# Kernel tuning notes

Hardware: AMD Instinct MI355X
Metric: run time of the kernel (lower is better)

Reference implementation:

```python
import jax, jax.numpy as jnp
import numpy as np

B, S, H = 2, 1024, 1024
NH, NKV, DH = 16, 4, 64
I, E, TOPK = 4096, 8, 2
EPS = 1e-5
ROPE_THETA = 10000.0


def setup_inputs() -> dict:
    key = jax.random.key(0)
    ks = jax.random.split(key, 16)
    std = 0.02
    inp = {
        'hidden_states': jax.random.normal(ks[0], (B, S, H), jnp.float32),
        'attention_mask': jnp.ones((B, S), jnp.int32),
        'position_ids': jnp.broadcast_to(jnp.arange(S, dtype=jnp.int32), (B, S)),
        'q_w': jax.random.normal(ks[1], (H, NH * DH), jnp.float32) * std,
        'k_w': jax.random.normal(ks[2], (H, NKV * DH), jnp.float32) * std,
        'v_w': jax.random.normal(ks[3], (H, NKV * DH), jnp.float32) * std,
        'o_w': jax.random.normal(ks[4], (NH * DH, H), jnp.float32) * std,
        'pre_attn_scale': jnp.ones((H,), jnp.float32),
        'post_attn_scale': jnp.ones((H,), jnp.float32),
        'pre_moe_scale': jnp.ones((H,), jnp.float32),
        'post_moe_scale': jnp.ones((H,), jnp.float32),
        'gate_w': jax.random.normal(ks[5], (H, E), jnp.float32) * std,
        'w_in': jax.random.normal(ks[6], (E, H, I), jnp.float32) * std,
        'w_v': jax.random.normal(ks[7], (E, H, I), jnp.float32) * std,
        'w_out': jax.random.normal(ks[8], (E, I, H), jnp.float32) * std,
    }
    return inp


def _rmsnorm(x, scale):
    var = jnp.mean(jnp.square(x), axis=-1, keepdims=True)
    return x * jax.lax.rsqrt(var + EPS) * scale


def _rope(x, positions):
    # x: [B, S, nheads, DH]; rotate-half RoPE
    half = DH // 2
    inv_freq = 1.0 / (ROPE_THETA ** (jnp.arange(0, half, dtype=jnp.float32) / half))
    ang = positions.astype(jnp.float32)[..., None] * inv_freq  # [B,S,half]
    cos = jnp.cos(ang)[:, :, None, :]
    sin = jnp.sin(ang)[:, :, None, :]
    x1, x2 = x[..., :half], x[..., half:]
    return jnp.concatenate([x1 * cos - x2 * sin, x2 * cos + x1 * sin], axis=-1)


def _attention(x, attention_mask, position_ids, q_w, k_w, v_w, o_w):
    q = (x @ q_w).reshape(B, S, NH, DH)
    k = (x @ k_w).reshape(B, S, NKV, DH)
    v = (x @ v_w).reshape(B, S, NKV, DH)
    q = _rope(q, position_ids)
    k = _rope(k, position_ids)
    groups = NH // NKV
    k = jnp.repeat(k, groups, axis=2)  # [B,S,NH,DH]
    v = jnp.repeat(v, groups, axis=2)
    scale = DH ** -0.5
    scores = jnp.einsum('bqhd,bkhd->bhqk', q, k) * scale
    causal = jnp.tril(jnp.ones((S, S), bool))
    valid = causal[None, None] & (attention_mask[:, None, None, :] > 0)
    scores = jnp.where(valid, scores, jnp.float32(-1e9))
    probs = jax.nn.softmax(scores, axis=-1)
    out = jnp.einsum('bhqk,bkhd->bqhd', probs, v).reshape(B, S, NH * DH)
    return out @ o_w


def _moe(x, gate_w, w_in, w_v, w_out):
    xf = x.reshape(-1, H)  # [T,H]
    T = xf.shape[0]
    logits = xf @ gate_w  # [T,E]
    probs = jax.nn.softmax(logits, axis=-1)
    top_w, top_i = jax.lax.top_k(probs, TOPK)  # Grok-1: no renormalization
    cw = jnp.zeros((T, E), xf.dtype).at[jnp.arange(T)[:, None], top_i].add(top_w)
    out = jnp.zeros_like(xf)
    for e in range(E):  # fixed small loop over experts
        h = jax.nn.gelu(xf @ w_in[e]) * (xf @ w_v[e])
        out = out + cw[:, e:e + 1] * (h @ w_out[e])
    return out.reshape(x.shape)


def reference(hidden_states, attention_mask, position_ids, q_w, k_w, v_w, o_w,
              pre_attn_scale, post_attn_scale, pre_moe_scale, post_moe_scale,
              gate_w, w_in, w_v, w_out):
    h = _rmsnorm(hidden_states, pre_attn_scale)
    attn = _attention(h, attention_mask, position_ids, q_w, k_w, v_w, o_w)
    attn = _rmsnorm(attn, post_attn_scale)
    x = hidden_states + attn
    h2 = _rmsnorm(x, pre_moe_scale)
    moe = _moe(h2, gate_w, w_in, w_v, w_out)
    moe = _rmsnorm(moe, post_moe_scale)
    return x + moe
```

## Files before the change

kernel.cpp:

```cpp
#include <hip/hip_runtime.h>
#include <hip/hip_bf16.h>
#include <math.h>

namespace {

constexpr int BB=2, SS=1024, HH=1024, NH=16, NKV=4, DH=64;
constexpr int II=4096, EE=8;
constexpr int TT=BB*SS;
constexpr int QKV=1536;
constexpr float EPS=1e-5f;

typedef __bf16 bf16x8 __attribute__((ext_vector_type(8)));
typedef float f32x4 __attribute__((ext_vector_type(4)));

__device__ __forceinline__ unsigned short f2bf(float x){
  union { float f; unsigned u; } un; un.f = x;
  unsigned r = un.u + 0x7fffu + ((un.u>>16)&1u);
  return (unsigned short)(r>>16);
}
__device__ __forceinline__ float bfval(unsigned short h){
  union { unsigned u; float f; } r; r.u = ((unsigned)h)<<16; return r.f;
}
__device__ __forceinline__ void split2(float v, unsigned short& hi, unsigned short& lo){
  hi = f2bf(v);
  lo = f2bf(v - bfval(hi));
}

__device__ __forceinline__ void gl_lds16(const void* g, void* l){
  __builtin_amdgcn_global_load_lds(
    (const __attribute__((address_space(1))) unsigned int*)g,
    (__attribute__((address_space(3))) unsigned int*)l, 16, 0, 0);
}

__device__ __forceinline__ float gelu_tanh(float x){
  float x3 = x*x*x;
  return 0.5f*x*(1.f + tanhf(0.7978845608028654f*(x + 0.044715f*x3)));
}

__global__ void rmsnorm_kernel(const float* __restrict__ in, const float* __restrict__ scale,
                               float* __restrict__ outf, unsigned short* __restrict__ outb,
                               unsigned short* __restrict__ outh, unsigned short* __restrict__ outl){
  int row = blockIdx.x, tid = threadIdx.x;
  const float* x = in + (size_t)row*HH;
  float ss = 0.f;
  for (int i=tid;i<HH;i+=256){ float v=x[i]; ss+=v*v; }
  __shared__ float red[256];
  red[tid]=ss; __syncthreads();
  for (int s=128;s>0;s>>=1){ if(tid<s) red[tid]+=red[tid+s]; __syncthreads(); }
  float inv = rsqrtf(red[0]/(float)HH + EPS);
  for (int i=tid;i<HH;i+=256){
    float v = x[i]*inv*scale[i];
    size_t o = (size_t)row*HH+i;
    if (outf) outf[o]=v;
    if (outb) outb[o]=f2bf(v);
    if (outh){ unsigned short h,l; split2(v,h,l); outh[o]=h; outl[o]=l; }
  }
}

__global__ void fuse_attn_post(const float* __restrict__ ao_raw, const float* __restrict__ hidden,
                               const float* __restrict__ post_scale, const float* __restrict__ pre_scale,
                               float* __restrict__ xb, float* __restrict__ hn,
                               unsigned short* __restrict__ hnb){
  int row = blockIdx.x, tid = threadIdx.x;
  const float* a = ao_raw + (size_t)row*HH;
  const float* h = hidden + (size_t)row*HH;
  float av[4], hv[4];
  float ss = 0.f;
#pragma unroll
  for (int i=0;i<4;i++){
    int idx = tid + i*256;
    av[i]=a[idx]; hv[i]=h[idx];
    ss += av[i]*av[i];
  }
  __shared__ float red[256];
  red[tid]=ss; __syncthreads();
  for (int s=128;s>0;s>>=1){ if(tid<s) red[tid]+=red[tid+s]; __syncthreads(); }
  float inv1 = rsqrtf(red[0]/(float)HH + EPS);
  __syncthreads();
  float xv[4]; float ss2=0.f;
#pragma unroll
  for (int i=0;i<4;i++){
    int idx = tid + i*256;
    xv[i] = hv[i] + av[i]*inv1*post_scale[idx];
    ss2 += xv[i]*xv[i];
  }
  red[tid]=ss2; __syncthreads();
  for (int s=128;s>0;s>>=1){ if(tid<s) red[tid]+=red[tid+s]; __syncthreads(); }
  float inv2 = rsqrtf(red[0]/(float)HH + EPS);
#pragma unroll
  for (int i=0;i<4;i++){
    int idx = tid + i*256;
    size_t o = (size_t)row*HH + idx;
    xb[o] = xv[i];
    float v = xv[i]*inv2*pre_scale[idx];
    hn[o] = v;
    hnb[o] = f2bf(v);
  }
}

__global__ void fuse_moe_post(const float* __restrict__ moe, const float* __restrict__ xb,
                              const float* __restrict__ scale, float* __restrict__ out){
  int row = blockIdx.x, tid = threadIdx.x;
  const float* m = moe + (size_t)row*HH;
  float mv[4]; float ss=0.f;
#pragma unroll
  for (int i=0;i<4;i++){
    int idx = tid + i*256;
    mv[i]=m[idx]; ss += mv[i]*mv[i];
  }
  __shared__ float red[256];
  red[tid]=ss; __syncthreads();
  for (int s=128;s>0;s>>=1){ if(tid<s) red[tid]+=red[tid+s]; __syncthreads(); }
  float inv = rsqrtf(red[0]/(float)HH + EPS);
#pragma unroll
  for (int i=0;i<4;i++){
    int idx = tid + i*256;
    size_t o = (size_t)row*HH + idx;
    out[o] = xb[o] + mv[i]*inv*scale[idx];
  }
}

__global__ void rope_split_kernel(const float* __restrict__ x, int stride, int off,
                                  const int* __restrict__ pos_ids,
                                  unsigned short* __restrict__ oh, unsigned short* __restrict__ ol,
                                  int nheads){
  int idx = blockIdx.x*256 + threadIdx.x;
  int total = TT*nheads*32;
  if (idx >= total) return;
  int j = idx & 31;
  int hh = (idx>>5) % nheads;
  int t = idx / (32*nheads);
  float pos = (float)pos_ids[t];
  float inv_freq = powf(10000.f, -(float)j/32.f);
  float ang = pos * inv_freq;
  float s, c; sincosf(ang, &s, &c);
  const float* p = x + (size_t)t*stride + off + hh*DH;
  float x1 = p[j], x2 = p[j+32];
  float r1 = x1*c - x2*s;
  float r2 = x2*c + x1*s;
  size_t o = ((size_t)t*nheads + hh)*DH;
  unsigned short h1,l1,h2,l2;
  split2(r1,h1,l1); split2(r2,h2,l2);
  oh[o+j]=h1;    ol[o+j]=l1;
  oh[o+j+32]=h2; ol[o+j+32]=l2;
}

__global__ __launch_bounds__(256) void vt_split_kernel(const float* __restrict__ src, int stride, int off,
    unsigned short* __restrict__ vth, unsigned short* __restrict__ vtl){
  int k0 = blockIdx.x*64;
  int kvh = blockIdx.y;
  int b = blockIdx.z;
  __shared__ float tile[64][65];
  int t = threadIdx.x;
  int c4 = (t&15)*4, gg = t>>4;
#pragma unroll
  for (int r=0;r<4;r++){
    int kk = gg + r*16;
    float4 v = *reinterpret_cast<const float4*>(src + (size_t)(b*SS+k0+kk)*stride + off + kvh*DH + c4);
    tile[kk][c4]=v.x; tile[kk][c4+1]=v.y; tile[kk][c4+2]=v.z; tile[kk][c4+3]=v.w;
  }
  __syncthreads();
#pragma unroll
  for (int r=0;r<4;r++){
    int dd = gg + r*16;
    ushort4 h4, l4v;
    split2(tile[c4  ][dd], h4.x, l4v.x);
    split2(tile[c4+1][dd], h4.y, l4v.y);
    split2(tile[c4+2][dd], h4.z, l4v.z);
    split2(tile[c4+3][dd], h4.w, l4v.w);
    size_t o = ((size_t)(b*NKV+kvh)*DH + dd)*SS + k0 + c4;
    *reinterpret_cast<ushort4*>(vth+o)=h4;
    *reinterpret_cast<ushort4*>(vtl+o)=l4v;
  }
}

__global__ __launch_bounds__(256) void attn_mfma(
    const unsigned short* __restrict__ qh, const unsigned short* __restrict__ ql,
    const unsigned short* __restrict__ khp, const unsigned short* __restrict__ klp,
    const unsigned short* __restrict__ vth, const unsigned short* __restrict__ vtl,
    const int* __restrict__ amask,
    unsigned short* __restrict__ ctxh, unsigned short* __restrict__ ctxl)
{
  int qb = blockIdx.x, h = blockIdx.y, b = blockIdx.z;
  int kvh = h >> 2;
  int tid = threadIdx.x;
  int w = tid >> 6, lane = tid & 63;
  int g = lane >> 4, l15 = lane & 15;

  __shared__ __align__(16) unsigned short Klh[64*64];
  __shared__ __align__(16) unsigned short Kll[64*64];
  __shared__ __align__(16) unsigned short Vlh[64*64];
  __shared__ __align__(16) unsigned short Vll[64*64];
  __shared__ __align__(16) unsigned short Pst[4][2][16*72];

  int q0w = qb*64 + w*16;

  bf16x8 qfh[2], qfl[2];
  {
    size_t qrow = ((size_t)(b*SS + q0w + l15)*NH + h)*DH;
#pragma unroll
    for (int ks=0; ks<2; ks++){
      qfh[ks] = *reinterpret_cast<const bf16x8*>(qh + qrow + ks*32 + g*8);
      qfl[ks] = *reinterpret_cast<const bf16x8*>(ql + qrow + ks*32 + g*8);
    }
  }

  f32x4 acc[4];
  float m_run[4], l_run[4];
#pragma unroll
  for (int i=0;i<4;i++){ acc[i]=f32x4{0,0,0,0}; m_run[i]=-1e30f; l_run[i]=0.f; }

  int nkv = qb + 1;
  for (int kblk=0; kblk<nkv; kblk++){
    int k0 = kblk*64;
    __syncthreads();
#pragma unroll
    for (int shot=0; shot<2; shot++){
      int a = shot*256 + tid;
      int row = a>>3, seg = a&7;
      int ss8 = (seg ^ (row&7))*8;
      int lo = row*64 + seg*8;
      size_t kg = ((size_t)(b*SS + k0 + row)*NKV + kvh)*DH + ss8;
      size_t vg = ((size_t)(b*NKV + kvh)*DH + row)*SS + k0 + ss8;
      gl_lds16(khp + kg, Klh + lo);
      gl_lds16(klp + kg, Kll + lo);
      gl_lds16(vth + vg, Vlh + lo);
      gl_lds16(vtl + vg, Vll + lo);
    }
    __syncthreads();

    f32x4 sf[4];
#pragma unroll
    for (int nf=0;nf<4;nf++) sf[nf]=f32x4{0,0,0,0};
#pragma unroll
    for (int ks=0; ks<2; ks++){
#pragma unroll
      for (int nf=0; nf<4; nf++){
        int krow = nf*16 + l15;
        int off = krow*64 + (((ks*4+g) ^ (krow&7))*8);
        bf16x8 bh = *reinterpret_cast<const bf16x8*>(Klh + off);
        bf16x8 bl = *reinterpret_cast<const bf16x8*>(Kll + off);
        sf[nf] = __builtin_amdgcn_mfma_f32_16x16x32_bf16(qfh[ks], bh, sf[nf],0,0,0);
        sf[nf] = __builtin_amdgcn_mfma_f32_16x16x32_bf16(qfh[ks], bl, sf[nf],0,0,0);
        sf[nf] = __builtin_amdgcn_mfma_f32_16x16x32_bf16(qfl[ks], bh, sf[nf],0,0,0);
      }
    }

    int am4[4];
#pragma unroll
    for (int nf=0;nf<4;nf++) am4[nf] = amask[b*SS + k0 + nf*16 + l15];
#pragma unroll
    for (int nf=0;nf<4;nf++){
      int k_abs = k0 + nf*16 + l15;
#pragma unroll
      for (int r=0;r<4;r++){
        float s = sf[nf][r]*0.125f;
        int q_abs = q0w + g*4 + r;
        if (k_abs > q_abs || am4[nf] <= 0) s = -1e9f;
        sf[nf][r] = s;
      }
    }

    float m_new[4], fsc[4];
#pragma unroll
    for (int r=0;r<4;r++){
      float v = fmaxf(fmaxf(sf[0][r],sf[1][r]), fmaxf(sf[2][r],sf[3][r]));
#pragma unroll
      for (int o=1;o<16;o<<=1) v = fmaxf(v, __shfl_xor(v,o));
      m_new[r] = fmaxf(m_run[r], v);
      fsc[r] = expf(m_run[r] - m_new[r]);
      m_run[r] = m_new[r];
    }

    unsigned short* Ph  = Pst[w][0];
    unsigned short* Plo = Pst[w][1];
    float rsum[4] = {0.f,0.f,0.f,0.f};
#pragma unroll
    for (int nf=0;nf<4;nf++){
#pragma unroll
      for (int r=0;r<4;r++){
        float p = expf(sf[nf][r] - m_new[r]);
        rsum[r] += p;
        unsigned short hi = f2bf(p);
        float lo = p - bfval(hi);
        Ph [(g*4+r)*72 + nf*16 + l15] = hi;
        Plo[(g*4+r)*72 + nf*16 + l15] = f2bf(lo);
      }
    }
#pragma unroll
    for (int r=0;r<4;r++){
#pragma unroll
      for (int o=1;o<16;o<<=1) rsum[r] += __shfl_xor(rsum[r],o);
      l_run[r] = l_run[r]*fsc[r] + rsum[r];
#pragma unroll
      for (int nf=0;nf<4;nf++) acc[nf][r] *= fsc[r];
    }

#pragma unroll
    for (int ks=0; ks<2; ks++){
      bf16x8 pa = *reinterpret_cast<const bf16x8*>(Ph  + l15*72 + ks*32 + g*8);
      bf16x8 pl = *reinterpret_cast<const bf16x8*>(Plo + l15*72 + ks*32 + g*8);
#pragma unroll
      for (int nf=0; nf<4; nf++){
        int drow = nf*16 + l15;
        int off = drow*64 + (((ks*4+g) ^ (drow&7))*8);
        bf16x8 vh = *reinterpret_cast<const bf16x8*>(Vlh + off);
        bf16x8 vl = *reinterpret_cast<const bf16x8*>(Vll + off);
        acc[nf] = __builtin_amdgcn_mfma_f32_16x16x32_bf16(pa, vh, acc[nf],0,0,0);
        acc[nf] = __builtin_amdgcn_mfma_f32_16x16x32_bf16(pa, vl, acc[nf],0,0,0);
        acc[nf] = __builtin_amdgcn_mfma_f32_16x16x32_bf16(pl, vh, acc[nf],0,0,0);
      }
    }
  }

#pragma unroll
  for (int r=0;r<4;r++){
    float inv = 1.f / l_run[r];
    size_t orow = ((size_t)(b*SS + q0w + g*4 + r)*NH + h)*DH;
#pragma unroll
    for (int nf=0;nf<4;nf++){
      float v = acc[nf][r]*inv;
      unsigned short hi,lo; split2(v,hi,lo);
      ctxh[orow + nf*16 + l15] = hi;
      ctxl[orow + nf*16 + l15] = lo;
    }
  }
}

__global__ void route_kernel(const float* __restrict__ x, const float* __restrict__ gw,
                             int* __restrict__ counts, int* __restrict__ lists,
                             float* __restrict__ cw){
  int t = blockIdx.x;
  int lane = threadIdx.x;
  float acc[EE];
#pragma unroll
  for (int e=0;e<EE;e++) acc[e]=0.f;
  for (int hh=lane; hh<HH; hh+=64){
    float xv = x[(size_t)t*HH + hh];
#pragma unroll
    for (int e=0;e<EE;e++) acc[e] += xv*gw[hh*EE+e];
  }
#pragma unroll
  for (int e=0;e<EE;e++){
#pragma unroll
    for (int off=1; off<64; off<<=1) acc[e] += __shfl_xor(acc[e], off);
  }
  if (lane==0){
    float m = acc[0];
    for (int e=1;e<EE;e++) m = fmaxf(m, acc[e]);
    float p[EE], s=0.f;
    for (int e=0;e<EE;e++){ p[e]=expf(acc[e]-m); s+=p[e]; }
    float invs = 1.f/s;
    for (int e=0;e<EE;e++) p[e]*=invs;
    int i1=0;
    for (int e=1;e<EE;e++) if (p[e]>p[i1]) i1=e;
    int i2 = (i1==0)?1:0;
    for (int e=0;e<EE;e++) if (e!=i1 && p[e]>p[i2]) i2=e;
    int pos = atomicAdd(&counts[i1],1);
    lists[i1*TT+pos]=t; cw[i1*TT+pos]=p[i1];
    pos = atomicAdd(&counts[i2],1);
    lists[i2*TT+pos]=t; cw[i2*TT+pos]=p[i2];
  }
}

__global__ void prefix_kernel(const int* __restrict__ c, int* __restrict__ b,
                              const float* __restrict__ cw, float* __restrict__ cw_slot){
  int lane = threadIdx.x;
  __shared__ int sb[EE+1];
  if (lane==0){
    int s=0;
    for (int e=0;e<EE;e++){ sb[e]=s; b[e]=s; s+=c[e]; }
    sb[EE]=s; b[EE]=s;
  }
  __syncthreads();
  for (int e=0;e<EE;e++){
    int cnt=c[e], base=sb[e];
    for (int i=lane;i<cnt;i+=64) cw_slot[base+i]=cw[e*TT+i];
  }
}

__global__ void moe_combine(const unsigned short* __restrict__ t0,
                            const unsigned short* __restrict__ t1,
                            const float* __restrict__ cwslot,
                            const int* __restrict__ ntotp,
                            unsigned short* __restrict__ ehb){
  int row = blockIdx.x;
  if (row >= *ntotp) return;
  float c = cwslot[row];
  size_t base = (size_t)row*II;
  int tid = threadIdx.x;
  for (int c0 = tid*8; c0 < II; c0 += 256*8){
    ushort4 x0 = *reinterpret_cast<const ushort4*>(t0+base+c0);
    ushort4 x1 = *reinterpret_cast<const ushort4*>(t0+base+c0+4);
    ushort4 y0 = *reinterpret_cast<const ushort4*>(t1+base+c0);
    ushort4 y1 = *reinterpret_cast<const ushort4*>(t1+base+c0+4);
    ushort4 o0, o1;
    o0.x = f2bf(gelu_tanh(bfval(x0.x))*bfval(y0.x)*c);
    o0.y = f2bf(gelu_tanh(bfval(x0.y))*bfval(y0.y)*c);
    o0.z = f2bf(gelu_tanh(bfval(x0.z))*bfval(y0.z)*c);
    o0.w = f2bf(gelu_tanh(bfval(x0.w))*bfval(y0.w)*c);
    o1.x = f2bf(gelu_tanh(bfval(x1.x))*bfval(y1.x)*c);
    o1.y = f2bf(gelu_tanh(bfval(x1.y))*bfval(y1.y)*c);
    o1.z = f2bf(gelu_tanh(bfval(x1.z))*bfval(y1.z)*c);
    o1.w = f2bf(gelu_tanh(bfval(x1.w))*bfval(y1.w)*c);
    *reinterpret_cast<ushort4*>(ehb+base+c0)   = o0;
    *reinterpret_cast<ushort4*>(ehb+base+c0+4) = o1;
  }
}

__global__ __launch_bounds__(256) void transpose_cvt(const float* __restrict__ in,
    unsigned short* __restrict__ out, int K, int N, size_t in_zstride, size_t out_zstride){
  __shared__ float tile[64][65];
  int k0 = blockIdx.x*64, n0 = blockIdx.y*64;
  const float* inz = in + in_zstride*blockIdx.z;
  unsigned short* outz = out + out_zstride*blockIdx.z;
  int t = threadIdx.x;
  int c4 = (t&15)*4, g = t>>4;
#pragma unroll
  for (int r=0;r<4;r++){
    int kk = g + r*16;
    float4 v = *reinterpret_cast<const float4*>(inz + (size_t)(k0+kk)*N + n0 + c4);
    tile[kk][c4]=v.x; tile[kk][c4+1]=v.y; tile[kk][c4+2]=v.z; tile[kk][c4+3]=v.w;
  }
  __syncthreads();
#pragma unroll
  for (int r=0;r<4;r++){
    int nn = g + r*16;
    ushort4 o;
    o.x=f2bf(tile[c4][nn]);   o.y=f2bf(tile[c4+1][nn]);
    o.z=f2bf(tile[c4+2][nn]); o.w=f2bf(tile[c4+3][nn]);
    *reinterpret_cast<ushort4*>(outz + (size_t)(n0+nn)*K + k0 + c4) = o;
  }
}

__global__ __launch_bounds__(256) void transpose_cvt_split(const float* __restrict__ in,
    unsigned short* __restrict__ oh, unsigned short* __restrict__ ol, int K, int N){
  __shared__ float tile[64][65];
  int k0 = blockIdx.x*64, n0 = blockIdx.y*64;
  int t = threadIdx.x;
  int c4 = (t&15)*4, g = t>>4;
#pragma unroll
  for (int r=0;r<4;r++){
    int kk = g + r*16;
    float4 v = *reinterpret_cast<const float4*>(in + (size_t)(k0+kk)*N + n0 + c4);
    tile[kk][c4]=v.x; tile[kk][c4+1]=v.y; tile[kk][c4+2]=v.z; tile[kk][c4+3]=v.w;
  }
  __syncthreads();
#pragma unroll
  for (int r=0;r<4;r++){
    int nn = g + r*16;
    ushort4 h4, l4v;
    split2(tile[c4  ][nn], h4.x, l4v.x);
    split2(tile[c4+1][nn], h4.y, l4v.y);
    split2(tile[c4+2][nn], h4.z, l4v.z);
    split2(tile[c4+3][nn], h4.w, l4v.w);
    size_t o = (size_t)(n0+nn)*K + k0 + c4;
    *reinterpret_cast<ushort4*>(oh + o) = h4;
    *reinterpret_cast<ushort4*>(ol + o) = l4v;
  }
}

__global__ __launch_bounds__(256,2) void mgemm_split(
    const unsigned short* __restrict__ Ah, const unsigned short* __restrict__ Alo,
    const unsigned short* __restrict__ Bh, const unsigned short* __restrict__ Blo,
    float* __restrict__ Cf, int NY, int N, int K)
{
  int bid = blockIdx.x;
  int qq = bid >> 7, rr = bid & 127;
  int xti = rr >> 3, sbit = rr & 7;
  int g = qq*8 + sbit;
  if (g >= NY) return;
  int row0 = xti*128, col0 = g*128;
  __shared__ __align__(16) unsigned short lds[32768];

  int t = threadIdx.x;
  int lane = t&63, w = t>>6, wr = w>>1, wc = w&1;
  int sr = t>>2, seg = t&3;
  int swzs = (t>>3)&3;

  f32x4 acc[4][4];
#pragma unroll
  for (int m=0;m<4;m++)
#pragma unroll
    for (int n=0;n<4;n++) acc[m][n]=f32x4{0,0,0,0};

  int l15 = lane&15, l4 = lane>>4;
  int swzr = (l15>>1)&3;

  auto stage = [&](int buf, int k0){
    unsigned short* Lb = lds + buf*16384;
    int ksw = (seg ^ swzs)*8;
#pragma unroll
    for (int i=0;i<2;i++){
      int ldso = (sr + i*64)*32 + seg*8;
      size_t ar = (size_t)(row0 + sr + i*64);
      size_t br = (size_t)(col0 + sr + i*64);
      gl_lds16(Ah  + ar*K + k0 + ksw, Lb +         ldso);
      gl_lds16(Alo + ar*K + k0 + ksw, Lb + 4096  + ldso);
      gl_lds16(Bh  + br*K + k0 + ksw, Lb + 8192  + ldso);
      gl_lds16(Blo + br*K + k0 + ksw, Lb + 12288 + ldso);
    }
  };

  stage(0, 0);
  __syncthreads();
  int cur = 0;
  int NIT = K/32;
  int cofs = (l4 ^ swzr)*8;
  for (int it=0; it<NIT; it++){
    if (it+1 < NIT) stage(cur^1, (it+1)*32);
    const unsigned short* Lb = lds + cur*16384;
    bf16x8 ah[4], al[4], bh[4], bl[4];
#pragma unroll
    for (int m=0;m<4;m++){
      int ro = (wr*64 + m*16 + l15)*32 + cofs;
      ah[m]=*reinterpret_cast<const bf16x8*>(Lb +        ro);
      al[m]=*reinterpret_cast<const bf16x8*>(Lb + 4096 + ro);
    }
#pragma unroll
    for (int n=0;n<4;n++){
      int ro = (wc*64 + n*16 + l15)*32 + cofs;
      bh[n]=*reinterpret_cast<const bf16x8*>(Lb + 8192  + ro);
      bl[n]=*reinterpret_cast<const bf16x8*>(Lb + 12288 + ro);
    }
#pragma unroll
    for (int m=0;m<4;m++)
#pragma unroll
      for (int n=0;n<4;n++){
        acc[m][n] = __builtin_amdgcn_mfma_f32_16x16x32_bf16(ah[m], bh[n], acc[m][n], 0,0,0);
        acc[m][n] = __builtin_amdgcn_mfma_f32_16x16x32_bf16(ah[m], bl[n], acc[m][n], 0,0,0);
        acc[m][n] = __builtin_amdgcn_mfma_f32_16x16x32_bf16(al[m], bh[n], acc[m][n], 0,0,0);
      }
    __syncthreads();
    cur ^= 1;
  }

#pragma unroll
  for (int m=0;m<4;m++){
    int rb = wr*64 + m*16 + l4*4;
#pragma unroll
    for (int n=0;n<4;n++){
      int col = col0 + wc*64 + n*16 + l15;
#pragma unroll
      for (int r=0;r<4;r++){
        int row = row0 + rb + r;
        Cf[(size_t)row*N + col] = acc[m][n][r];
      }
    }
  }
}

__global__ __launch_bounds__(256,2) void mgemm_up(
    const unsigned short* __restrict__ A, const unsigned short* __restrict__ B0b,
    const unsigned short* __restrict__ B1b, size_t bstride,
    unsigned short* __restrict__ Cb0, unsigned short* __restrict__ Cb1,
    const int* __restrict__ listb,
    const int* __restrict__ countb, const int* __restrict__ basep)
{
  int bid = blockIdx.x;
  int qq = bid >> 7, rr = bid & 127;
  int xti = rr >> 3, sbit = rr & 7;
  int g = qq*8 + sbit;
  int y = g & 31, e = g >> 5;

  int M = countb[e];
  int row0 = xti*128;
  if (row0 >= M) return;
  int which = y & 1;
  int col0 = (y >> 1)*256;
  const unsigned short* B = (which ? B1b : B0b) + bstride*e;
  int slot = basep[e];
  const int* rowlist = listb + e*TT;

  __shared__ __align__(16) unsigned short lds[3][12288];

  int t = threadIdx.x;
  int lane = t&63, w = t>>6;
  int sr = t>>2, seg = t&3;
  int swzs = (t>>3)&3;

  size_t arow[2], brow[4];
#pragma unroll
  for (int i=0;i<2;i++){
    int r = row0 + sr + i*64;
    int rc = (r < M) ? r : (M-1);
    arow[i] = (size_t)rowlist[rc];
  }
#pragma unroll
  for (int i=0;i<4;i++)
    brow[i] = (size_t)(col0 + sr + i*64);

  f32x4 acc[8][4];
#pragma unroll
  for (int m=0;m<8;m++)
#pragma unroll
    for (int n=0;n<4;n++) acc[m][n]=f32x4{0,0,0,0};

  int l15 = lane&15, l4 = lane>>4;
  int cofs = (l4 ^ ((l15>>1)&3))*8;

  auto stage = [&](int buf, int k0){
    int ksw = (seg ^ swzs)*8;
#pragma unroll
    for (int i=0;i<2;i++){
      int ldso = (sr + i*64)*32 + seg*8;
      gl_lds16(A + arow[i]*HH + k0 + ksw, &lds[buf][0] + ldso);
    }
#pragma unroll
    for (int i=0;i<4;i++){
      int ldso = 4096 + (sr + i*64)*32 + seg*8;
      gl_lds16(B + brow[i]*HH + k0 + ksw, &lds[buf][0] + ldso);
    }
  };

  constexpr int NIT = HH/32;
  stage(0, 0);
  stage(1, 32);

  for (int it=0; it<NIT; it++){
    if (it+1 < NIT) asm volatile("s_waitcnt vmcnt(6)" ::: "memory");
    else            asm volatile("s_waitcnt vmcnt(0)" ::: "memory");
    __builtin_amdgcn_s_barrier();
    if (it+2 < NIT) stage((it+2)%3, (it+2)*32);

    const unsigned short* La = &lds[it%3][0];
    const unsigned short* Lb = La + 4096;
    bf16x8 af[8], bf[4];
#pragma unroll
    for (int m=0;m<8;m++)
      af[m] = *reinterpret_cast<const bf16x8*>(La + (m*16 + l15)*32 + cofs);
#pragma unroll
    for (int n=0;n<4;n++)
      bf[n] = *reinterpret_cast<const bf16x8*>(Lb + (w*64 + n*16 + l15)*32 + cofs);
#pragma unroll
    for (int m=0;m<8;m++)
#pragma unroll
      for (int n=0;n<4;n++)
        acc[m][n] = __builtin_amdgcn_mfma_f32_16x16x32_bf16(af[m], bf[n], acc[m][n], 0,0,0);
  }

  unsigned short* Cb = which ? Cb1 : Cb0;
#pragma unroll
  for (int m=0;m<8;m++){
    int rb = m*16 + l4*4;
#pragma unroll
    for (int n=0;n<4;n++){
      int col = col0 + w*64 + n*16 + l15;
#pragma unroll
      for (int r=0;r<4;r++){
        int row = row0 + rb + r;
        if (row >= M) continue;
        Cb[(size_t)(slot+row)*II + col] = f2bf(acc[m][n][r]);
      }
    }
  }
}

__global__ __launch_bounds__(256,3) void mgemm_down(
    const unsigned short* __restrict__ A, const unsigned short* __restrict__ B0b,
    size_t bstride, float* __restrict__ Cf,
    const int* __restrict__ listb,
    const int* __restrict__ countb, const int* __restrict__ basep)
{
  int bid = blockIdx.x;
  int qq = bid >> 7, rr = bid & 127;
  int xti = rr >> 3, sbit = rr & 7;
  int g = qq*8 + sbit;
  int y = g & 15, e = g >> 4;

  int M = countb[e];
  int row0 = xti*128;
  if (row0 >= M) return;
  int col0 = (y & 7)*128;
  int kbase = (y >> 3)*(II/2);
  int KL = II/2;
  const unsigned short* B = B0b + bstride*e;
  int slot = basep[e];
  const int* rowlist = listb + e*TT;

  __shared__ __align__(16) unsigned short lds[3][2][4096];

  int t = threadIdx.x;
  int lane = t&63, w = t>>6, wr = w>>1, wc = w&1;
  int sr = t>>2, seg = t&3;
  int swzs = (t>>3)&3;

  size_t arow[2], brow[2];
#pragma unroll
  for (int i=0;i<2;i++){
    int r = row0 + sr + i*64;
    int rc = (r < M) ? r : (M-1);
    arow[i] = (size_t)(slot + rc);
    brow[i] = (size_t)(col0 + sr + i*64);
  }

  f32x4 acc[4][4];
#pragma unroll
  for (int m=0;m<4;m++)
#pragma unroll
    for (int n=0;n<4;n++) acc[m][n]=f32x4{0,0,0,0};

  int l15 = lane&15, l4 = lane>>4;
  int cofs = (l4 ^ ((l15>>1)&3))*8;

  auto stage = [&](int buf, int k0){
    int ksw = (seg ^ swzs)*8;
#pragma unroll
    for (int i=0;i<2;i++){
      int ldso = (sr + i*64)*32 + seg*8;
      gl_lds16(A + arow[i]*II + kbase + k0 + ksw, &lds[buf][0][0] + ldso);
      gl_lds16(B + brow[i]*II + kbase + k0 + ksw, &lds[buf][1][0] + ldso);
    }
  };

  int NIT = KL/32;
  stage(0, 0);
  stage(1, 32);

  for (int it=0; it<NIT; it++){
    if (it+1 < NIT) asm volatile("s_waitcnt vmcnt(4)" ::: "memory");
    else            asm volatile("s_waitcnt vmcnt(0)" ::: "memory");
    __builtin_amdgcn_s_barrier();
    if (it+2 < NIT) stage((it+2)%3, (it+2)*32);

    int cb = it%3;
    const unsigned short* La = &lds[cb][0][0];
    const unsigned short* Lb = &lds[cb][1][0];
    bf16x8 af[4], bf[4];
#pragma unroll
    for (int m=0;m<4;m++)
      af[m] = *reinterpret_cast<const bf16x8*>(La + (wr*64 + m*16 + l15)*32 + cofs);
#pragma unroll
    for (int n=0;n<4;n++)
      bf[n] = *reinterpret_cast<const bf16x8*>(Lb + (wc*64 + n*16 + l15)*32 + cofs);
#pragma unroll
    for (int m=0;m<4;m++)
#pragma unroll
      for (int n=0;n<4;n++)
        acc[m][n] = __builtin_amdgcn_mfma_f32_16x16x32_bf16(af[m], bf[n], acc[m][n], 0,0,0);
  }

#pragma unroll
  for (int m=0;m<4;m++){
    int rb = wr*64 + m*16 + l4*4;
#pragma unroll
    for (int n=0;n<4;n++){
      int col = col0 + wc*64 + n*16 + l15;
#pragma unroll
      for (int r=0;r<4;r++){
        int row = row0 + rb + r;
        if (row >= M) continue;
        atomicAdd(&Cf[(size_t)rowlist[row]*HH + col], acc[m][n][r]);
      }
    }
  }
}

}

extern "C" void kernel_launch(void* const* d_in, const int* in_sizes, int n_in,
                              void* d_out, int out_size, void* d_ws, size_t ws_size,
                              hipStream_t stream) {
  const float* hidden = (const float*)d_in[0];
  const int*   mask   = (const int*)d_in[1];
  const int*   pos    = (const int*)d_in[2];
  const float* q_w    = (const float*)d_in[3];
  const float* k_w    = (const float*)d_in[4];
  const float* v_w    = (const float*)d_in[5];
  const float* o_w    = (const float*)d_in[6];
  const float* pre_attn_scale  = (const float*)d_in[7];
  const float* post_attn_scale = (const float*)d_in[8];
  const float* pre_moe_scale   = (const float*)d_in[9];
  const float* post_moe_scale  = (const float*)d_in[10];
  const float* gate_w = (const float*)d_in[11];
  const float* w_in   = (const float*)d_in[12];
  const float* w_v    = (const float*)d_in[13];
  const float* w_out  = (const float*)d_in[14];
  float* out = (float*)d_out;

  char* base = (char*)d_ws;
  auto carve = [&](size_t bytes)->char*{
    char* r = base; base += (bytes + 255) & ~(size_t)255; return r;
  };
  float* hn  = (float*)carve((size_t)TT*HH*4);
  unsigned short* hnb = (unsigned short*)carve((size_t)TT*HH*2);
  unsigned short* hnh = (unsigned short*)carve((size_t)TT*HH*2);
  unsigned short* hnl = (unsigned short*)carve((size_t)TT*HH*2);
  float* qkvb = (float*)carve((size_t)TT*QKV*4);
  unsigned short* qsh = (unsigned short*)carve((size_t)TT*NH*DH*2);
  unsigned short* qsl = (unsigned short*)carve((size_t)TT*NH*DH*2);
  unsigned short* ksh = (unsigned short*)carve((size_t)TT*NKV*DH*2);
  unsigned short* ksl = (unsigned short*)carve((size_t)TT*NKV*DH*2);
  unsigned short* vth = (unsigned short*)carve((size_t)TT*NKV*DH*2);
  unsigned short* vtl = (unsigned short*)carve((size_t)TT*NKV*DH*2);
  unsigned short* ctxh = (unsigned short*)carve((size_t)TT*NH*DH*2);
  unsigned short* ctxl = (unsigned short*)carve((size_t)TT*NH*DH*2);
  float* ao  = (float*)carve((size_t)TT*HH*4);
  float* xb  = (float*)carve((size_t)TT*HH*4);
  float* moe = (float*)carve((size_t)TT*HH*4);
  float* cw  = (float*)carve((size_t)EE*TT*4);
  float* cw_slot = (float*)carve((size_t)2*TT*4);
  int* counts = (int*)carve(64*4);
  int* bases  = (int*)carve(64*4);
  int* lists  = (int*)carve((size_t)EE*TT*4);
  unsigned short* qkvwTh = (unsigned short*)carve((size_t)QKV*HH*2);
  unsigned short* qkvwTl = (unsigned short*)carve((size_t)QKV*HH*2);
  unsigned short* owTh = (unsigned short*)carve((size_t)NH*DH*HH*2);
  unsigned short* owTl = (unsigned short*)carve((size_t)NH*DH*HH*2);
  unsigned short* ehb   = (unsigned short*)carve((size_t)2*TT*II*2);
  unsigned short* tmp0  = (unsigned short*)carve((size_t)2*TT*II*2);
  unsigned short* tmp1  = (unsigned short*)carve((size_t)2*TT*II*2);
  unsigned short* winT  = (unsigned short*)carve((size_t)EE*II*HH*2);
  unsigned short* wvT   = (unsigned short*)carve((size_t)EE*II*HH*2);
  unsigned short* woutT = (unsigned short*)carve((size_t)EE*HH*II*2);
  size_t estride = (size_t)II*HH;

  rmsnorm_kernel<<<TT,256,0,stream>>>(hidden, pre_attn_scale, nullptr, nullptr, hnh, hnl);
  transpose_cvt_split<<<dim3(16,16),256,0,stream>>>(q_w, qkvwTh, qkvwTl, HH, NH*DH);
  transpose_cvt_split<<<dim3(16,4), 256,0,stream>>>(k_w, qkvwTh + (size_t)1024*HH, qkvwTl + (size_t)1024*HH, HH, NKV*DH);
  transpose_cvt_split<<<dim3(16,4), 256,0,stream>>>(v_w, qkvwTh + (size_t)1280*HH, qkvwTl + (size_t)1280*HH, HH, NKV*DH);
  transpose_cvt_split<<<dim3(16,16),256,0,stream>>>(o_w, owTh, owTl, NH*DH, HH);

  mgemm_split<<<2*128,256,0,stream>>>(hnh, hnl, qkvwTh, qkvwTl, qkvb, QKV/128, QKV, HH);

  rope_split_kernel<<<(TT*NH*32+255)/256,256,0,stream>>>(qkvb, QKV, 0, pos, qsh, qsl, NH);
  rope_split_kernel<<<(TT*NKV*32+255)/256,256,0,stream>>>(qkvb, QKV, 1024, pos, ksh, ksl, NKV);
  vt_split_kernel<<<dim3(SS/64,NKV,BB),256,0,stream>>>(qkvb, QKV, 1280, vth, vtl);

  attn_mfma<<<dim3(SS/64,NH,BB),256,0,stream>>>(qsh, qsl, ksh, ksl, vth, vtl, mask, ctxh, ctxl);

  mgemm_split<<<128,256,0,stream>>>(ctxh, ctxl, owTh, owTl, ao, HH/128, HH, NH*DH);
  fuse_attn_post<<<TT,256,0,stream>>>(ao, hidden, post_attn_scale, pre_moe_scale, xb, hn, hnb);

  hipMemsetAsync(counts, 0, 64*sizeof(int), stream);
  hipMemsetAsync(moe, 0, (size_t)TT*HH*sizeof(float), stream);
  route_kernel<<<TT,64,0,stream>>>(hn, gate_w, counts, lists, cw);
  prefix_kernel<<<1,64,0,stream>>>(counts, bases, cw, cw_slot);

  transpose_cvt<<<dim3(16,64,EE),256,0,stream>>>(w_in, winT, HH, II, (size_t)HH*II, estride);
  transpose_cvt<<<dim3(16,64,EE),256,0,stream>>>(w_v,  wvT,  HH, II, (size_t)HH*II, estride);
  transpose_cvt<<<dim3(64,16,EE),256,0,stream>>>(w_out, woutT, II, HH, (size_t)II*HH, estride);

  mgemm_up<<<16*32*EE,256,0,stream>>>(hnb, winT, wvT, estride, tmp0, tmp1,
      lists, counts, bases);
  moe_combine<<<2*TT,256,0,stream>>>(tmp0, tmp1, cw_slot, bases+EE, ehb);
  mgemm_down<<<16*16*EE,256,0,stream>>>(ehb, woutT, estride, moe,
      lists, counts, bases);

  fuse_moe_post<<<TT,256,0,stream>>>(moe, xb, post_moe_scale, out);
}
```

Before: 602.8 us.

## Fuse GELU-gate combine into MoE up-projection GEMM epilogue

The MoE up-projection GEMM now computes both the w_in and w_v products for the same 128x128 tile in one block, keeping two accumulator sets. Its epilogue applies gelu(a)*b*routing weight and writes ehb directly. This removes the separate moe_combine kernel, the two bf16 intermediate buffers, and the cw_slot compaction step. In exchange the per-thread accumulators double and the tile shape changes from 128x256 to 128x128 per output, which may hurt occupancy or MFMA reuse.

```diff
diff --git a/kernel.cpp b/kernel.cpp
--- a/kernel.cpp
+++ b/kernel.cpp
@@ -363,48 +363,11 @@
   }
 }
 
-__global__ void prefix_kernel(const int* __restrict__ c, int* __restrict__ b,
-                              const float* __restrict__ cw, float* __restrict__ cw_slot){
-  int lane = threadIdx.x;
-  __shared__ int sb[EE+1];
-  if (lane==0){
+__global__ void prefix_kernel(const int* __restrict__ c, int* __restrict__ b){
+  if (threadIdx.x==0){
     int s=0;
-    for (int e=0;e<EE;e++){ sb[e]=s; b[e]=s; s+=c[e]; }
-    sb[EE]=s; b[EE]=s;
-  }
-  __syncthreads();
-  for (int e=0;e<EE;e++){
-    int cnt=c[e], base=sb[e];
-    for (int i=lane;i<cnt;i+=64) cw_slot[base+i]=cw[e*TT+i];
-  }
-}
-
-__global__ void moe_combine(const unsigned short* __restrict__ t0,
-                            const unsigned short* __restrict__ t1,
-                            const float* __restrict__ cwslot,
-                            const int* __restrict__ ntotp,
-                            unsigned short* __restrict__ ehb){
-  int row = blockIdx.x;
-  if (row >= *ntotp) return;
-  float c = cwslot[row];
-  size_t base = (size_t)row*II;
-  int tid = threadIdx.x;
-  for (int c0 = tid*8; c0 < II; c0 += 256*8){
-    ushort4 x0 = *reinterpret_cast<const ushort4*>(t0+base+c0);
-    ushort4 x1 = *reinterpret_cast<const ushort4*>(t0+base+c0+4);
-    ushort4 y0 = *reinterpret_cast<const ushort4*>(t1+base+c0);
-    ushort4 y1 = *reinterpret_cast<const ushort4*>(t1+base+c0+4);
-    ushort4 o0, o1;
-    o0.x = f2bf(gelu_tanh(bfval(x0.x))*bfval(y0.x)*c);
-    o0.y = f2bf(gelu_tanh(bfval(x0.y))*bfval(y0.y)*c);
-    o0.z = f2bf(gelu_tanh(bfval(x0.z))*bfval(y0.z)*c);
-    o0.w = f2bf(gelu_tanh(bfval(x0.w))*bfval(y0.w)*c);
-    o1.x = f2bf(gelu_tanh(bfval(x1.x))*bfval(y1.x)*c);
-    o1.y = f2bf(gelu_tanh(bfval(x1.y))*bfval(y1.y)*c);
-    o1.z = f2bf(gelu_tanh(bfval(x1.z))*bfval(y1.z)*c);
-    o1.w = f2bf(gelu_tanh(bfval(x1.w))*bfval(y1.w)*c);
-    *reinterpret_cast<ushort4*>(ehb+base+c0)   = o0;
-    *reinterpret_cast<ushort4*>(ehb+base+c0+4) = o1;
+    for (int e=0;e<EE;e++){ b[e]=s; s+=c[e]; }
+    b[EE]=s;
   }
 }
 
@@ -553,8 +516,8 @@
 __global__ __launch_bounds__(256,2) void mgemm_up(
     const unsigned short* __restrict__ A, const unsigned short* __restrict__ B0b,
     const unsigned short* __restrict__ B1b, size_t bstride,
-    unsigned short* __restrict__ Cb0, unsigned short* __restrict__ Cb1,
-    const int* __restrict__ listb,
+    unsigned short* __restrict__ ehb,
+    const int* __restrict__ listb, const float* __restrict__ cwb,
     const int* __restrict__ countb, const int* __restrict__ basep)
 {
   int bid = blockIdx.x;
@@ -566,35 +529,34 @@
   int M = countb[e];
   int row0 = xti*128;
   if (row0 >= M) return;
-  int which = y & 1;
-  int col0 = (y >> 1)*256;
-  const unsigned short* B = (which ? B1b : B0b) + bstride*e;
+  int col0 = y*128;
+  const unsigned short* B0 = B0b + bstride*e;
+  const unsigned short* B1 = B1b + bstride*e;
   int slot = basep[e];
   const int* rowlist = listb + e*TT;
-
-  __shared__ __align__(16) unsigned short lds[3][12288];
+  const float* cwp = cwb + e*TT;
+
+  __shared__ __align__(16) unsigned short lds[3][3][4096];
 
   int t = threadIdx.x;
-  int lane = t&63, w = t>>6;
+  int lane = t&63, w = t>>6, wr = w>>1, wc = w&1;
   int sr = t>>2, seg = t&3;
   int swzs = (t>>3)&3;
 
-  size_t arow[2], brow[4];
+  size_t arow[2], brow[2];
 #pragma unroll
   for (int i=0;i<2;i++){
     int r = row0 + sr + i*64;
     int rc = (r < M) ? r : (M-1);
     arow[i] = (size_t)rowlist[rc];
-  }
-#pragma unroll
-  for (int i=0;i<4;i++)
     brow[i] = (size_t)(col0 + sr + i*64);
-
-  f32x4 acc[8][4];
-#pragma unroll
-  for (int m=0;m<8;m++)
-#pragma unroll
-    for (int n=0;n<4;n++) acc[m][n]=f32x4{0,0,0,0};
+  }
+
+  f32x4 acc0[4][4], acc1[4][4];
+#pragma unroll
+  for (int m=0;m<4;m++)
+#pragma unroll
+    for (int n=0;n<4;n++){ acc0[m][n]=f32x4{0,0,0,0}; acc1[m][n]=f32x4{0,0,0,0}; }
 
   int l15 = lane&15, l4 = lane>>4;
   int cofs = (l4 ^ ((l15>>1)&3))*8;
@@ -604,12 +566,9 @@
 #pragma unroll
     for (int i=0;i<2;i++){
       int ldso = (sr + i*64)*32 + seg*8;
-      gl_lds16(A + arow[i]*HH + k0 + ksw, &lds[buf][0] + ldso);
-    }
-#pragma unroll
-    for (int i=0;i<4;i++){
-      int ldso = 4096 + (sr + i*64)*32 + seg*8;
-      gl_lds16(B + brow[i]*HH + k0 + ksw, &lds[buf][0] + ldso);
+      gl_lds16(A  + arow[i]*HH + k0 + ksw, &lds[buf][0][0] + ldso);
+      gl_lds16(B0 + brow[i]*HH + k0 + ksw, &lds[buf][1][0] + ldso);
+      gl_lds16(B1 + brow[i]*HH + k0 + ksw, &lds[buf][2][0] + ldso);
     }
   };
 
@@ -623,34 +582,41 @@
     __builtin_amdgcn_s_barrier();
     if (it+2 < NIT) stage((it+2)%3, (it+2)*32);
 
-    const unsigned short* La = &lds[it%3][0];
-    const unsigned short* Lb = La + 4096;
-    bf16x8 af[8], bf[4];
-#pragma unroll
-    for (int m=0;m<8;m++)
-      af[m] = *reinterpret_cast<const bf16x8*>(La + (m*16 + l15)*32 + cofs);
-#pragma unroll
-    for (int n=0;n<4;n++)
-      bf[n] = *reinterpret_cast<const bf16x8*>(Lb + (w*64 + n*16 + l15)*32 + cofs);
-#pragma unroll
-    for (int m=0;m<8;m++)
-#pragma unroll
-      for (int n=0;n<4;n++)
-        acc[m][n] = __builtin_amdgcn_mfma_f32_16x16x32_bf16(af[m], bf[n], acc[m][n], 0,0,0);
-  }
-
-  unsigned short* Cb = which ? Cb1 : Cb0;
-#pragma unroll
-  for (int m=0;m<8;m++){
-    int rb = m*16 + l4*4;
+    int cb = it%3;
+    const unsigned short* La  = &lds[cb][0][0];
+    const unsigned short* Lb0 = &lds[cb][1][0];
+    const unsigned short* Lb1 = &lds[cb][2][0];
+    bf16x8 af[4], b0f[4], b1f[4];
+#pragma unroll
+    for (int m=0;m<4;m++)
+      af[m] = *reinterpret_cast<const bf16x8*>(La + (wr*64 + m*16 + l15)*32 + cofs);
 #pragma unroll
     for (int n=0;n<4;n++){
-      int col = col0 + w*64 + n*16 + l15;
+      int ro = (wc*64 + n*16 + l15)*32 + cofs;
+      b0f[n] = *reinterpret_cast<const bf16x8*>(Lb0 + ro);
+      b1f[n] = *reinterpret_cast<const bf16x8*>(Lb1 + ro);
+    }
+#pragma unroll
+    for (int m=0;m<4;m++)
+#pragma unroll
+      for (int n=0;n<4;n++){
+        acc0[m][n] = __builtin_amdgcn_mfma_f32_16x16x32_bf16(af[m], b0f[n], acc0[m][n], 0,0,0);
+        acc1[m][n] = __builtin_amdgcn_mfma_f32_16x16x32_bf16(af[m], b1f[n], acc1[m][n], 0,0,0);
+      }
+  }
+
+#pragma unroll
+  for (int m=0;m<4;m++){
+    int rb = wr*64 + m*16 + l4*4;
+#pragma unroll
+    for (int n=0;n<4;n++){
+      int col = col0 + wc*64 + n*16 + l15;
 #pragma unroll
       for (int r=0;r<4;r++){
         int row = row0 + rb + r;
         if (row >= M) continue;
-        Cb[(size_t)(slot+row)*II + col] = f2bf(acc[m][n][r]);
+        float v = gelu_tanh(acc0[m][n][r]) * acc1[m][n][r] * cwp[row];
+        ehb[(size_t)(slot+row)*II + col] = f2bf(v);
       }
     }
   }
@@ -799,7 +765,6 @@
   float* xb  = (float*)carve((size_t)TT*HH*4);
   float* moe = (float*)carve((size_t)TT*HH*4);
   float* cw  = (float*)carve((size_t)EE*TT*4);
-  float* cw_slot = (float*)carve((size_t)2*TT*4);
   int* counts = (int*)carve(64*4);
   int* bases  = (int*)carve(64*4);
   int* lists  = (int*)carve((size_t)EE*TT*4);
@@ -808,8 +773,6 @@
   unsigned short* owTh = (unsigned short*)carve((size_t)NH*DH*HH*2);
   unsigned short* owTl = (unsigned short*)carve((size_t)NH*DH*HH*2);
   unsigned short* ehb   = (unsigned short*)carve((size_t)2*TT*II*2);
-  unsigned short* tmp0  = (unsigned short*)carve((size_t)2*TT*II*2);
-  unsigned short* tmp1  = (unsigned short*)carve((size_t)2*TT*II*2);
   unsigned short* winT  = (unsigned short*)carve((size_t)EE*II*HH*2);
   unsigned short* wvT   = (unsigned short*)carve((size_t)EE*II*HH*2);
   unsigned short* woutT = (unsigned short*)carve((size_t)EE*HH*II*2);
@@ -835,15 +798,14 @@
   hipMemsetAsync(counts, 0, 64*sizeof(int), stream);
   hipMemsetAsync(moe, 0, (size_t)TT*HH*sizeof(float), stream);
   route_kernel<<<TT,64,0,stream>>>(hn, gate_w, counts, lists, cw);
-  prefix_kernel<<<1,64,0,stream>>>(counts, bases, cw, cw_slot);
+  prefix_kernel<<<1,64,0,stream>>>(counts, bases);
 
   transpose_cvt<<<dim3(16,64,EE),256,0,stream>>>(w_in, winT, HH, II, (size_t)HH*II, estride);
   transpose_cvt<<<dim3(16,64,EE),256,0,stream>>>(w_v,  wvT,  HH, II, (size_t)HH*II, estride);
   transpose_cvt<<<dim3(64,16,EE),256,0,stream>>>(w_out, woutT, II, HH, (size_t)II*HH, estride);
 
-  mgemm_up<<<16*32*EE,256,0,stream>>>(hnb, winT, wvT, estride, tmp0, tmp1,
-      lists, counts, bases);
-  moe_combine<<<2*TT,256,0,stream>>>(tmp0, tmp1, cw_slot, bases+EE, ehb);
+  mgemm_up<<<16*32*EE,256,0,stream>>>(hnb, winT, wvT, estride, ehb,
+      lists, cw, counts, bases);
   mgemm_down<<<16*16*EE,256,0,stream>>>(ehb, woutT, estride, moe,
       lists, counts, bases);
 
```

Result: no change. 610.1 us (+1.2%).
